# Optimization experiments

Measured on AMD Instinct MI355X. Metric: run time of the kernel, lower is better.

## Reference

```python
import jax, jax.numpy as jnp
import numpy as np

THETA = 10000.0


def apply_rope(t):
    """Partial rotary on first head_dim//2 dims, interleaved pairs (rotary_embedding_torch).
    t: (B, H, S, D) float32."""
    B, H, S, D = t.shape
    rot_dim = D // 2  # RotaryEmbedding(head_dim // 2)
    inv_freq = 1.0 / (THETA ** (jnp.arange(0, rot_dim, 2, dtype=jnp.float32) / rot_dim))  # (rot_dim//2,)
    pos = jnp.arange(S, dtype=jnp.float32)
    freqs = pos[:, None] * inv_freq[None, :]            # (S, rot_dim//2)
    freqs = jnp.repeat(freqs, 2, axis=-1)               # (S, rot_dim) interleaved
    cos, sin = jnp.cos(freqs), jnp.sin(freqs)           # (S, rot_dim)
    t_rot, t_pass = t[..., :rot_dim], t[..., rot_dim:]
    x1 = t_rot[..., 0::2]
    x2 = t_rot[..., 1::2]
    rot_half = jnp.stack((-x2, x1), axis=-1).reshape(t_rot.shape)
    t_rot = t_rot * cos + rot_half * sin
    return jnp.concatenate([t_rot, t_pass], axis=-1)


def setup_inputs() -> dict:
    key = jax.random.key(0)
    k1, k2, k3, k4, k5 = jax.random.split(key, 5)
    B, S, Dm = 2, 2048, 1024
    scale = 1.0 / np.sqrt(Dm)
    return {
        "x": jax.random.normal(k1, (B, S, Dm), dtype=jnp.float32),
        "Wqkv": jax.random.normal(k2, (3 * Dm, Dm), dtype=jnp.float32) * scale,
        "bqkv": jax.random.normal(k3, (3 * Dm,), dtype=jnp.float32) * 0.01,
        "Wout": jax.random.normal(k4, (Dm, Dm), dtype=jnp.float32) * scale,
        "bout": jax.random.normal(k5, (Dm,), dtype=jnp.float32) * 0.01,
    }


def reference(x, Wqkv, bqkv, Wout, bout):
    B, S, Dm = x.shape
    H = 16
    Dh = Dm // H
    qkv = x @ Wqkv.T + bqkv                              # (B, S, 3*Dm)
    qkv = qkv.reshape(B, S, 3, H, Dh).transpose(2, 0, 3, 1, 4)  # (3, B, H, S, Dh)
    q, k, v = qkv[0], qkv[1], qkv[2]
    q = apply_rope(q.astype(jnp.float32))
    k = apply_rope(k.astype(jnp.float32))
    scores = jnp.einsum("bhqd,bhkd->bhqk", q, k) / jnp.sqrt(jnp.float32(Dh))
    attn = jax.nn.softmax(scores, axis=-1)
    out = jnp.einsum("bhqk,bhkd->bhqd", attn, v)         # (B, H, S, Dh)
    out = out.transpose(0, 2, 1, 3).reshape(B, S, Dm)
    return out @ Wout.T + bout
```

## Files before the change

kernel.cpp:

```cpp
#include <hip/hip_runtime.h>

#define S_LEN 2048
#define DMODEL 1024
#define NHEAD 16
#define DHEAD 64
#define BATCH 2
#define BH_TOT (BATCH * NHEAD)
#define TOK (BATCH * S_LEN)
#define NQKV (3 * DMODEL)

#define QSCALE 0.18033688011112042f

typedef float  f32x4  __attribute__((ext_vector_type(4)));
typedef float  f32x16 __attribute__((ext_vector_type(16)));
typedef int    i32x4  __attribute__((ext_vector_type(4)));
typedef unsigned u32x2 __attribute__((ext_vector_type(2)));
typedef __bf16 bf16x8 __attribute__((ext_vector_type(8)));
typedef __bf16 bf16x4 __attribute__((ext_vector_type(4)));
typedef __bf16 bf16x2 __attribute__((ext_vector_type(2)));

typedef __attribute__((address_space(1))) void* as1_ptr;
typedef __attribute__((address_space(3))) void* as3_ptr;

__device__ __forceinline__ void gl2lds16(const void* g, void* l) {
  __builtin_amdgcn_global_load_lds((as1_ptr)(void*)g, (as3_ptr)l, 16, 0, 0);
}

__device__ __forceinline__ f32x4 mfma32(bf16x8 a, bf16x8 b, f32x4 c) {
  return __builtin_amdgcn_mfma_f32_16x16x32_bf16(a, b, c, 0, 0, 0);
}

__device__ __forceinline__ f32x16 mfma3216(bf16x8 a, bf16x8 b, f32x16 c) {
  return __builtin_amdgcn_mfma_f32_32x32x16_bf16(a, b, c, 0, 0, 0);
}

__device__ __forceinline__ unsigned pack2(float a, float b) {
  bf16x2 t;
  t[0] = (__bf16)a;
  t[1] = (__bf16)b;
  return __builtin_bit_cast(unsigned, t);
}

__device__ __forceinline__ bf16x8 pfragn(float a0, float a1, float a2, float a3,
                                         float a4, float a5, float a6, float a7) {
  const i32x4 w = {(int)pack2(a0, a1), (int)pack2(a2, a3),
                   (int)pack2(a4, a5), (int)pack2(a6, a7)};
  return __builtin_bit_cast(bf16x8, w);
}

__global__ __launch_bounds__(256) void cvt_kernel(const float* __restrict__ src,
                                                  __bf16* __restrict__ dst, int n) {
  const int i = (blockIdx.x * 256 + threadIdx.x) * 4;
  if (i >= n) return;
  const f32x4 v = *(const f32x4*)(src + i);
  bf16x4 o;
  o[0] = (__bf16)v[0]; o[1] = (__bf16)v[1]; o[2] = (__bf16)v[2]; o[3] = (__bf16)v[3];
  *(bf16x4*)(dst + i) = o;
}

__device__ __forceinline__ void gemm_tile_128(const __bf16* __restrict__ A,
                                              const __bf16* __restrict__ Bw,
                                              const int Kd, const int tileM, const int tileN,
                                              __bf16* As, __bf16* Bs, f32x4 acc[4][4]) {
  const int t    = threadIdx.x;
  const int lane = t & 63;
  const int wave = t >> 6;
  const int quad = lane >> 4;
  const int c    = lane & 15;
  const int wm   = (wave >> 1) << 6;
  const int wn   = (wave & 1) << 6;

  const int u0 = t, u1 = t + 256;
  const __bf16* gA0 = A  + (size_t)(tileM + (u0 >> 2)) * Kd + (u0 & 3) * 8;
  const __bf16* gA1 = A  + (size_t)(tileM + (u1 >> 2)) * Kd + (u1 & 3) * 8;
  const __bf16* gB0 = Bw + (size_t)(tileN + (u0 >> 2)) * Kd + (u0 & 3) * 8;
  const __bf16* gB1 = Bw + (size_t)(tileN + (u1 >> 2)) * Kd + (u1 & 3) * 8;
  __bf16* lA0 = As + u0 * 8; __bf16* lA1 = As + u1 * 8;
  __bf16* lB0 = Bs + u0 * 8; __bf16* lB1 = Bs + u1 * 8;

  for (int k0 = 0; k0 < Kd; k0 += 32) {
    gl2lds16(gA0 + k0, lA0);
    gl2lds16(gA1 + k0, lA1);
    gl2lds16(gB0 + k0, lB0);
    gl2lds16(gB1 + k0, lB1);
    __syncthreads();
    bf16x8 af[4], bfr[4];
#pragma unroll
    for (int mt = 0; mt < 4; ++mt)
      af[mt] = *(const bf16x8*)(As + (wm + mt * 16 + c) * 32 + quad * 8);
#pragma unroll
    for (int nt = 0; nt < 4; ++nt)
      bfr[nt] = *(const bf16x8*)(Bs + (wn + nt * 16 + c) * 32 + quad * 8);
#pragma unroll
    for (int mt = 0; mt < 4; ++mt)
#pragma unroll
      for (int nt = 0; nt < 4; ++nt)
        acc[mt][nt] = mfma32(af[mt], bfr[nt], acc[mt][nt]);
    __syncthreads();
  }
}

__global__ __launch_bounds__(256) void gemm_qkv_kernel(const __bf16* __restrict__ xb,
                                                       const __bf16* __restrict__ Wb,
                                                       const float* __restrict__ bias,
                                                       __bf16* __restrict__ Qb,
                                                       __bf16* __restrict__ Kb,
                                                       __bf16* __restrict__ Vtb) {
  __shared__ __align__(16) __bf16 As[128 * 32];
  __shared__ __align__(16) __bf16 Bs[128 * 32];
  f32x4 acc[4][4];
#pragma unroll
  for (int i = 0; i < 4; ++i)
#pragma unroll
    for (int j = 0; j < 4; ++j) acc[i][j] = (f32x4){0.f, 0.f, 0.f, 0.f};

  const int tileM = blockIdx.y * 128;
  const int tileN = blockIdx.x * 128;
  gemm_tile_128(xb, Wb, DMODEL, tileM, tileN, As, Bs, acc);

  const int t = threadIdx.x;
  const int lane = t & 63, wave = t >> 6;
  const int quad = lane >> 4, c = lane & 15;
  const int wm = (wave >> 1) << 6, wn = (wave & 1) << 6;

#pragma unroll
  for (int nt = 0; nt < 4; ++nt) {
    const int col = tileN + wn + nt * 16 + c;
    const float bv = bias[col];
    const int which = col >> 10;
    const int h  = (col >> 6) & 15;
    const int dh = col & 63;
    if (which == 2) {
#pragma unroll
      for (int mt = 0; mt < 4; ++mt) {
        const int row0 = tileM + wm + mt * 16 + quad * 4;
        const int bb = row0 >> 11;
        const int ss = row0 & (S_LEN - 1);
        bf16x4 o;
#pragma unroll
        for (int r = 0; r < 4; ++r) o[r] = (__bf16)(acc[mt][nt][r] + bv);
        *(bf16x4*)(Vtb + (((size_t)(bb * NHEAD + h)) * DHEAD + dh) * S_LEN + ss) = o;
      }
    } else {
      __bf16* dst = (which == 0) ? Qb : Kb;
      const float scl = (which == 0) ? QSCALE : 1.0f;
#pragma unroll
      for (int mt = 0; mt < 4; ++mt) {
#pragma unroll
        for (int r = 0; r < 4; ++r) {
          const int row = tileM + wm + mt * 16 + quad * 4 + r;
          const int bb = row >> 11;
          const int ss = row & (S_LEN - 1);
          dst[(((size_t)(bb * NHEAD + h)) * S_LEN + ss) * DHEAD + dh] =
              (__bf16)((acc[mt][nt][r] + bv) * scl);
        }
      }
    }
  }
}

__global__ __launch_bounds__(256) void gemm_out_kernel(const __bf16* __restrict__ AOb,
                                                       const __bf16* __restrict__ Wb,
                                                       const float* __restrict__ bout,
                                                       float* __restrict__ out) {
  __shared__ __align__(16) __bf16 As[128 * 32];
  __shared__ __align__(16) __bf16 Bs[128 * 32];
  f32x4 acc[4][4];
#pragma unroll
  for (int i = 0; i < 4; ++i)
#pragma unroll
    for (int j = 0; j < 4; ++j) acc[i][j] = (f32x4){0.f, 0.f, 0.f, 0.f};

  const int tileM = blockIdx.y * 128;
  const int tileN = blockIdx.x * 128;
  gemm_tile_128(AOb, Wb, DMODEL, tileM, tileN, As, Bs, acc);

  const int t = threadIdx.x;
  const int lane = t & 63, wave = t >> 6;
  const int quad = lane >> 4, c = lane & 15;
  const int wm = (wave >> 1) << 6, wn = (wave & 1) << 6;

#pragma unroll
  for (int nt = 0; nt < 4; ++nt) {
    const int col = tileN + wn + nt * 16 + c;
    const float bv = bout[col];
#pragma unroll
    for (int mt = 0; mt < 4; ++mt) {
#pragma unroll
      for (int r = 0; r < 4; ++r) {
        const int row = tileM + wm + mt * 16 + quad * 4 + r;
        out[(size_t)row * DMODEL + col] = acc[mt][nt][r] + bv;
      }
    }
  }
}

__global__ __launch_bounds__(256) void rope_kernel(__bf16* __restrict__ Qb, __bf16* __restrict__ Kb) {
  const int idx = blockIdx.x * 256 + threadIdx.x;
  const int j  = idx & 15;
  const int s  = (idx >> 4) & (S_LEN - 1);
  const int bh = (idx >> 15) & (BH_TOT - 1);
  __bf16* base = (idx >> 20) ? Kb : Qb;
  bf16x2* p = (bf16x2*)(base + ((size_t)bh * S_LEN + s) * DHEAD) + j;
  bf16x2 v = *p;
  const float x1 = (float)v[0];
  const float x2 = (float)v[1];
  const float LOG2_10000 = 13.287712379549449f;
  const float inv = exp2f(-(float)j * (LOG2_10000 / 16.0f));
  const float ang = (float)s * inv;
  float sn, cs;
  sincosf(ang, &sn, &cs);
  bf16x2 o;
  o[0] = (__bf16)(x1 * cs - x2 * sn);
  o[1] = (__bf16)(x2 * cs + x1 * sn);
  *p = o;
}

__global__ __launch_bounds__(128, 2) void attn_kernel(const __bf16* __restrict__ Qb,
                                                      const __bf16* __restrict__ Kb,
                                                      const __bf16* __restrict__ Vtb,
                                                      __bf16* __restrict__ AOb) {
  __shared__ __align__(16) __bf16 Ks[2][64 * 64];
  __shared__ __align__(16) __bf16 Vts[2][64 * 64];

  const int qt = blockIdx.x;
  const int bh = blockIdx.y;
  const int b = bh >> 4, h = bh & 15;
  const int t = threadIdx.x, wave = t >> 6, lane = t & 63;
  const int c31 = lane & 31, hi = lane >> 5;
  const int cx = c31 & 7;
  const size_t head = (size_t)bh * S_LEN * DHEAD;
  const int q0w = qt * 64 + wave * 32;

  bf16x8 qf[4];
#pragma unroll
  for (int s = 0; s < 4; ++s)
    qf[s] = *(const bf16x8*)(Qb + head + (size_t)(q0w + c31) * DHEAD + s * 16 + hi * 8);

  f32x16 zzero;
#pragma unroll
  for (int i = 0; i < 16; ++i) zzero[i] = 0.f;

  f32x16 ota[2], otb[2];
  ota[0] = zzero; ota[1] = zzero; otb[0] = zzero; otb[1] = zzero;
  float lp = 0.f;

  const __bf16* kg[4];
  const __bf16* vg[4];
  int loff[4];
#pragma unroll
  for (int i = 0; i < 4; ++i) {
    const int u = t + 128 * i;
    const int r = u >> 3, ch = (u & 7) ^ (r & 7);
    kg[i] = Kb + head + (size_t)r * DHEAD + ch * 8;
    vg[i] = Vtb + ((size_t)bh * DHEAD + r) * S_LEN + ch * 8;
    loff[i] = u * 8;
  }

#pragma unroll
  for (int i = 0; i < 4; ++i) {
    gl2lds16(kg[i], &Ks[0][loff[i]]);
    gl2lds16(vg[i], &Vts[0][loff[i]]);
  }

#define VREAD64(db, cb)                                                                   \
  __builtin_bit_cast(bf16x8, (i32x4){                                                     \
      (int)__builtin_bit_cast(u32x2, *(const bf16x4*)(&Vts[cur][((db)*32 + c31) * 64 +    \
                                  (((cb) ^ cx) * 8) + hi * 4]))[0],                       \
      (int)__builtin_bit_cast(u32x2, *(const bf16x4*)(&Vts[cur][((db)*32 + c31) * 64 +    \
                                  (((cb) ^ cx) * 8) + hi * 4]))[1],                       \
      (int)__builtin_bit_cast(u32x2, *(const bf16x4*)(&Vts[cur][((db)*32 + c31) * 64 +    \
                                  ((((cb) + 1) ^ cx) * 8) + hi * 4]))[0],                 \
      (int)__builtin_bit_cast(u32x2, *(const bf16x4*)(&Vts[cur][((db)*32 + c31) * 64 +    \
                                  ((((cb) + 1) ^ cx) * 8) + hi * 4]))[1]})

  for (int kb = 0; kb < S_LEN / 64; ++kb) {
    __syncthreads();
    const int cur = kb & 1;
    if (kb + 1 < S_LEN / 64) {
      const int nxt = cur ^ 1;
      const int k0n = (kb + 1) * 64;
#pragma unroll
      for (int i = 0; i < 4; ++i) {
        gl2lds16(kg[i] + (size_t)k0n * DHEAD, &Ks[nxt][loff[i]]);
        gl2lds16(vg[i] + k0n, &Vts[nxt][loff[i]]);
      }
    }

    bf16x8 kA0[4], kA1[4];
#pragma unroll
    for (int s = 0; s < 4; ++s) {
      kA0[s] = *(const bf16x8*)(&Ks[cur][c31 * 64 + (((s * 2 + hi) ^ cx) * 8)]);
      kA1[s] = *(const bf16x8*)(&Ks[cur][(32 + c31) * 64 + (((s * 2 + hi) ^ cx) * 8)]);
    }

    f32x16 z0 = zzero, z1 = zzero;
    __builtin_amdgcn_s_setprio(1);
#pragma unroll
    for (int s = 0; s < 4; ++s) {
      z0 = mfma3216(kA0[s], qf[s], z0);
      z1 = mfma3216(kA1[s], qf[s], z1);
    }
    __builtin_amdgcn_s_setprio(0);

    float p0[16], p1[16];
#pragma unroll
    for (int r = 0; r < 16; ++r) p0[r] = __builtin_amdgcn_exp2f(z0[r]);
#pragma unroll
    for (int r = 0; r < 16; ++r) p1[r] = __builtin_amdgcn_exp2f(z1[r]);

    lp += (((p0[0] + p0[1]) + (p0[2] + p0[3])) + ((p0[4] + p0[5]) + (p0[6] + p0[7])))
        + (((p0[8] + p0[9]) + (p0[10] + p0[11])) + ((p0[12] + p0[13]) + (p0[14] + p0[15])));
    lp += (((p1[0] + p1[1]) + (p1[2] + p1[3])) + ((p1[4] + p1[5]) + (p1[6] + p1[7])))
        + (((p1[8] + p1[9]) + (p1[10] + p1[11])) + ((p1[12] + p1[13]) + (p1[14] + p1[15])));

    __builtin_amdgcn_s_setprio(1);
    {
      const bf16x8 f0 = pfragn(p0[0], p0[1], p0[2], p0[3], p0[4], p0[5], p0[6], p0[7]);
      ota[0] = mfma3216(VREAD64(0, 0), f0, ota[0]);
      ota[1] = mfma3216(VREAD64(1, 0), f0, ota[1]);
      const bf16x8 f1 = pfragn(p0[8], p0[9], p0[10], p0[11], p0[12], p0[13], p0[14], p0[15]);
      otb[0] = mfma3216(VREAD64(0, 2), f1, otb[0]);
      otb[1] = mfma3216(VREAD64(1, 2), f1, otb[1]);
    }
    {
      const bf16x8 f0 = pfragn(p1[0], p1[1], p1[2], p1[3], p1[4], p1[5], p1[6], p1[7]);
      ota[0] = mfma3216(VREAD64(0, 4), f0, ota[0]);
      ota[1] = mfma3216(VREAD64(1, 4), f0, ota[1]);
      const bf16x8 f1 = pfragn(p1[8], p1[9], p1[10], p1[11], p1[12], p1[13], p1[14], p1[15]);
      otb[0] = mfma3216(VREAD64(0, 6), f1, otb[0]);
      otb[1] = mfma3216(VREAD64(1, 6), f1, otb[1]);
    }
    __builtin_amdgcn_s_setprio(0);
  }
#undef VREAD64

#pragma unroll
  for (int i = 0; i < 16; ++i) { ota[0][i] += otb[0][i]; ota[1][i] += otb[1][i]; }
  const float l = lp + __shfl_xor(lp, 32);
  const float inv = 1.0f / l;
  const int q = q0w + c31;
#pragma unroll
  for (int db = 0; db < 2; ++db) {
#pragma unroll
    for (int rg = 0; rg < 4; ++rg) {
      bf16x4 o;
#pragma unroll
      for (int i = 0; i < 4; ++i) o[i] = (__bf16)(ota[db][rg * 4 + i] * inv);
      const int d0 = db * 32 + rg * 8 + hi * 4;
      *(bf16x4*)(AOb + ((size_t)(b * S_LEN + q)) * DMODEL + h * DHEAD + d0) = o;
    }
  }
}

extern "C" void kernel_launch(void* const* d_in, const int* in_sizes, int n_in,
                              void* d_out, int out_size, void* d_ws, size_t ws_size,
                              hipStream_t stream) {
  const float* x    = (const float*)d_in[0];
  const float* Wqkv = (const float*)d_in[1];
  const float* bqkv = (const float*)d_in[2];
  const float* Wout = (const float*)d_in[3];
  const float* bout = (const float*)d_in[4];
  float* out = (float*)d_out;

  char* ws = (char*)d_ws;
  __bf16* xb    = (__bf16*)(ws + 0);
  __bf16* Wqkvb = (__bf16*)(ws + (size_t)8  * 1024 * 1024);
  __bf16* Woutb = (__bf16*)(ws + (size_t)14 * 1024 * 1024);
  __bf16* Qb    = (__bf16*)(ws + (size_t)16 * 1024 * 1024);
  __bf16* Kb    = (__bf16*)(ws + (size_t)24 * 1024 * 1024);
  __bf16* Vtb   = (__bf16*)(ws + (size_t)32 * 1024 * 1024);
  __bf16* AOb   = (__bf16*)(ws + (size_t)40 * 1024 * 1024);

  cvt_kernel<<<(TOK * DMODEL) / 1024, 256, 0, stream>>>(x, xb, TOK * DMODEL);
  cvt_kernel<<<(NQKV * DMODEL) / 1024, 256, 0, stream>>>(Wqkv, Wqkvb, NQKV * DMODEL);
  cvt_kernel<<<(DMODEL * DMODEL) / 1024, 256, 0, stream>>>(Wout, Woutb, DMODEL * DMODEL);

  gemm_qkv_kernel<<<dim3(NQKV / 128, TOK / 128), 256, 0, stream>>>(xb, Wqkvb, bqkv, Qb, Kb, Vtb);

  rope_kernel<<<(2 * BH_TOT * S_LEN * 16) / 256, 256, 0, stream>>>(Qb, Kb);

  attn_kernel<<<dim3(S_LEN / 64, BH_TOT), 128, 0, stream>>>(Qb, Kb, Vtb, AOb);

  gemm_out_kernel<<<dim3(DMODEL / 128, TOK / 128), 256, 0, stream>>>(AOb, Woutb, bout, out);
}
```

Measured before the change: 200.1 us.

## Restructure attention to single-wave blocks with 32-key tiles and no barriers

The attention kernel now runs one 64-thread wave per block over 32 queries, and processes keys in 32-row tiles instead of 64. Because each block is a single wave, __syncthreads is replaced by an explicit vmcnt wait, and the K and V fragments are read into registers before the next tile's async loads are issued into the other buffer. This removes cross-wave barrier stalls and doubles the number of blocks, which may improve latency hiding. The cost is half the K/V reuse per global load across queries, so L2 traffic doubles, along with more loop iterations and a new V swizzle pattern.

```diff
diff --git a/kernel.cpp b/kernel.cpp
--- a/kernel.cpp
+++ b/kernel.cpp
@@ -216,21 +216,22 @@
   *p = o;
 }
 
-__global__ __launch_bounds__(128, 2) void attn_kernel(const __bf16* __restrict__ Qb,
-                                                      const __bf16* __restrict__ Kb,
-                                                      const __bf16* __restrict__ Vtb,
-                                                      __bf16* __restrict__ AOb) {
-  __shared__ __align__(16) __bf16 Ks[2][64 * 64];
-  __shared__ __align__(16) __bf16 Vts[2][64 * 64];
+__global__ __launch_bounds__(64, 2) void attn_kernel(const __bf16* __restrict__ Qb,
+                                                     const __bf16* __restrict__ Kb,
+                                                     const __bf16* __restrict__ Vtb,
+                                                     __bf16* __restrict__ AOb) {
+  __shared__ __align__(16) __bf16 Ks[2][32 * 64];
+  __shared__ __align__(16) __bf16 Vts[2][64 * 32];
 
   const int qt = blockIdx.x;
   const int bh = blockIdx.y;
   const int b = bh >> 4, h = bh & 15;
-  const int t = threadIdx.x, wave = t >> 6, lane = t & 63;
+  const int lane = threadIdx.x & 63;
   const int c31 = lane & 31, hi = lane >> 5;
-  const int cx = c31 & 7;
+  const int cx7 = c31 & 7;
+  const int cxv = (c31 >> 1) & 3;
   const size_t head = (size_t)bh * S_LEN * DHEAD;
-  const int q0w = qt * 64 + wave * 32;
+  const int q0w = qt * 32;
 
   bf16x8 qf[4];
 #pragma unroll
@@ -247,93 +248,84 @@
 
   const __bf16* kg[4];
   const __bf16* vg[4];
-  int loff[4];
+  int lofK[4], lofV[4];
 #pragma unroll
   for (int i = 0; i < 4; ++i) {
-    const int u = t + 128 * i;
-    const int r = u >> 3, ch = (u & 7) ^ (r & 7);
-    kg[i] = Kb + head + (size_t)r * DHEAD + ch * 8;
-    vg[i] = Vtb + ((size_t)bh * DHEAD + r) * S_LEN + ch * 8;
-    loff[i] = u * 8;
+    const int u = lane + 64 * i;
+    const int rk = u >> 3, ck = (u & 7) ^ (rk & 7);
+    kg[i] = Kb + head + (size_t)rk * DHEAD + ck * 8;
+    lofK[i] = u * 8;
+    const int rv = u >> 2, cv = (u & 3) ^ ((rv >> 1) & 3);
+    vg[i] = Vtb + ((size_t)bh * DHEAD + rv) * S_LEN + cv * 8;
+    lofV[i] = u * 8;
   }
 
 #pragma unroll
   for (int i = 0; i < 4; ++i) {
-    gl2lds16(kg[i], &Ks[0][loff[i]]);
-    gl2lds16(vg[i], &Vts[0][loff[i]]);
-  }
-
-#define VREAD64(db, cb)                                                                   \
-  __builtin_bit_cast(bf16x8, (i32x4){                                                     \
-      (int)__builtin_bit_cast(u32x2, *(const bf16x4*)(&Vts[cur][((db)*32 + c31) * 64 +    \
-                                  (((cb) ^ cx) * 8) + hi * 4]))[0],                       \
-      (int)__builtin_bit_cast(u32x2, *(const bf16x4*)(&Vts[cur][((db)*32 + c31) * 64 +    \
-                                  (((cb) ^ cx) * 8) + hi * 4]))[1],                       \
-      (int)__builtin_bit_cast(u32x2, *(const bf16x4*)(&Vts[cur][((db)*32 + c31) * 64 +    \
-                                  ((((cb) + 1) ^ cx) * 8) + hi * 4]))[0],                 \
-      (int)__builtin_bit_cast(u32x2, *(const bf16x4*)(&Vts[cur][((db)*32 + c31) * 64 +    \
-                                  ((((cb) + 1) ^ cx) * 8) + hi * 4]))[1]})
-
-  for (int kb = 0; kb < S_LEN / 64; ++kb) {
-    __syncthreads();
-    const int cur = kb & 1;
-    if (kb + 1 < S_LEN / 64) {
-      const int nxt = cur ^ 1;
-      const int k0n = (kb + 1) * 64;
-#pragma unroll
-      for (int i = 0; i < 4; ++i) {
-        gl2lds16(kg[i] + (size_t)k0n * DHEAD, &Ks[nxt][loff[i]]);
-        gl2lds16(vg[i] + k0n, &Vts[nxt][loff[i]]);
-      }
-    }
-
-    bf16x8 kA0[4], kA1[4];
-#pragma unroll
-    for (int s = 0; s < 4; ++s) {
-      kA0[s] = *(const bf16x8*)(&Ks[cur][c31 * 64 + (((s * 2 + hi) ^ cx) * 8)]);
-      kA1[s] = *(const bf16x8*)(&Ks[cur][(32 + c31) * 64 + (((s * 2 + hi) ^ cx) * 8)]);
-    }
-
-    f32x16 z0 = zzero, z1 = zzero;
-    __builtin_amdgcn_s_setprio(1);
-#pragma unroll
-    for (int s = 0; s < 4; ++s) {
-      z0 = mfma3216(kA0[s], qf[s], z0);
-      z1 = mfma3216(kA1[s], qf[s], z1);
-    }
-    __builtin_amdgcn_s_setprio(0);
-
-    float p0[16], p1[16];
-#pragma unroll
-    for (int r = 0; r < 16; ++r) p0[r] = __builtin_amdgcn_exp2f(z0[r]);
-#pragma unroll
-    for (int r = 0; r < 16; ++r) p1[r] = __builtin_amdgcn_exp2f(z1[r]);
-
-    lp += (((p0[0] + p0[1]) + (p0[2] + p0[3])) + ((p0[4] + p0[5]) + (p0[6] + p0[7])))
-        + (((p0[8] + p0[9]) + (p0[10] + p0[11])) + ((p0[12] + p0[13]) + (p0[14] + p0[15])));
-    lp += (((p1[0] + p1[1]) + (p1[2] + p1[3])) + ((p1[4] + p1[5]) + (p1[6] + p1[7])))
-        + (((p1[8] + p1[9]) + (p1[10] + p1[11])) + ((p1[12] + p1[13]) + (p1[14] + p1[15])));
-
-    __builtin_amdgcn_s_setprio(1);
-    {
-      const bf16x8 f0 = pfragn(p0[0], p0[1], p0[2], p0[3], p0[4], p0[5], p0[6], p0[7]);
-      ota[0] = mfma3216(VREAD64(0, 0), f0, ota[0]);
-      ota[1] = mfma3216(VREAD64(1, 0), f0, ota[1]);
-      const bf16x8 f1 = pfragn(p0[8], p0[9], p0[10], p0[11], p0[12], p0[13], p0[14], p0[15]);
-      otb[0] = mfma3216(VREAD64(0, 2), f1, otb[0]);
-      otb[1] = mfma3216(VREAD64(1, 2), f1, otb[1]);
-    }
-    {
-      const bf16x8 f0 = pfragn(p1[0], p1[1], p1[2], p1[3], p1[4], p1[5], p1[6], p1[7]);
-      ota[0] = mfma3216(VREAD64(0, 4), f0, ota[0]);
-      ota[1] = mfma3216(VREAD64(1, 4), f0, ota[1]);
-      const bf16x8 f1 = pfragn(p1[8], p1[9], p1[10], p1[11], p1[12], p1[13], p1[14], p1[15]);
-      otb[0] = mfma3216(VREAD64(0, 6), f1, otb[0]);
-      otb[1] = mfma3216(VREAD64(1, 6), f1, otb[1]);
-    }
-    __builtin_amdgcn_s_setprio(0);
-  }
-#undef VREAD64
+    gl2lds16(kg[i], &Ks[0][lofK[i]]);
+    gl2lds16(vg[i], &Vts[0][lofV[i]]);
+  }
+
+#define VFRAG(CUR, db, kc)                                                                 \
+  __builtin_bit_cast(bf16x8, (i32x4){                                                      \
+      (int)__builtin_bit_cast(u32x2, *(const bf16x4*)(&Vts[CUR][((db) * 32 + c31) * 32 +   \
+                                     ((((kc) * 2) ^ cxv) * 8) + hi * 4]))[0],              \
+      (int)__builtin_bit_cast(u32x2, *(const bf16x4*)(&Vts[CUR][((db) * 32 + c31) * 32 +   \
+                                     ((((kc) * 2) ^ cxv) * 8) + hi * 4]))[1],              \
+      (int)__builtin_bit_cast(u32x2, *(const bf16x4*)(&Vts[CUR][((db) * 32 + c31) * 32 +   \
+                                     ((((kc) * 2 + 1) ^ cxv) * 8) + hi * 4]))[0],          \
+      (int)__builtin_bit_cast(u32x2, *(const bf16x4*)(&Vts[CUR][((db) * 32 + c31) * 32 +   \
+                                     ((((kc) * 2 + 1) ^ cxv) * 8) + hi * 4]))[1]})
+
+#define ATTN_TILE(KB, CUR)                                                                 \
+  {                                                                                        \
+    asm volatile("s_waitcnt vmcnt(0)" ::: "memory");                                       \
+    __builtin_amdgcn_sched_barrier(0);                                                     \
+    bf16x8 kA[4];                                                                          \
+    _Pragma("unroll")                                                                      \
+    for (int s = 0; s < 4; ++s)                                                            \
+      kA[s] = *(const bf16x8*)(&Ks[CUR][c31 * 64 + (((s * 2 + hi) ^ cx7) * 8)]);           \
+    const bf16x8 vA00 = VFRAG(CUR, 0, 0);                                                  \
+    const bf16x8 vA10 = VFRAG(CUR, 1, 0);                                                  \
+    const bf16x8 vA01 = VFRAG(CUR, 0, 1);                                                  \
+    const bf16x8 vA11 = VFRAG(CUR, 1, 1);                                                  \
+    __builtin_amdgcn_sched_barrier(0);                                                     \
+    if ((KB) + 1 < S_LEN / 32) {                                                           \
+      const int ka = ((KB) + 1) * (32 * DHEAD);                                            \
+      const int va = ((KB) + 1) * 32;                                                      \
+      _Pragma("unroll")                                                                    \
+      for (int i = 0; i < 4; ++i) {                                                        \
+        gl2lds16(kg[i] + ka, &Ks[(CUR) ^ 1][lofK[i]]);                                     \
+        gl2lds16(vg[i] + va, &Vts[(CUR) ^ 1][lofV[i]]);                                    \
+      }                                                                                    \
+    }                                                                                      \
+    __builtin_amdgcn_sched_barrier(0);                                                     \
+    f32x16 z = zzero;                                                                      \
+    __builtin_amdgcn_s_setprio(1);                                                         \
+    _Pragma("unroll")                                                                      \
+    for (int s = 0; s < 4; ++s) z = mfma3216(kA[s], qf[s], z);                             \
+    __builtin_amdgcn_s_setprio(0);                                                         \
+    float p[16];                                                                           \
+    _Pragma("unroll")                                                                      \
+    for (int r = 0; r < 16; ++r) p[r] = __builtin_amdgcn_exp2f(z[r]);                      \
+    lp += (((p[0] + p[1]) + (p[2] + p[3])) + ((p[4] + p[5]) + (p[6] + p[7])))              \
+        + (((p[8] + p[9]) + (p[10] + p[11])) + ((p[12] + p[13]) + (p[14] + p[15])));       \
+    const bf16x8 f0 = pfragn(p[0], p[1], p[2], p[3], p[4], p[5], p[6], p[7]);              \
+    const bf16x8 f1 = pfragn(p[8], p[9], p[10], p[11], p[12], p[13], p[14], p[15]);        \
+    __builtin_amdgcn_s_setprio(1);                                                         \
+    ota[0] = mfma3216(vA00, f0, ota[0]);                                                   \
+    ota[1] = mfma3216(vA10, f0, ota[1]);                                                   \
+    otb[0] = mfma3216(vA01, f1, otb[0]);                                                   \
+    otb[1] = mfma3216(vA11, f1, otb[1]);                                                   \
+    __builtin_amdgcn_s_setprio(0);                                                         \
+  }
+
+  for (int kbb = 0; kbb < S_LEN / 64; ++kbb) {
+    ATTN_TILE(2 * kbb, 0)
+    ATTN_TILE(2 * kbb + 1, 1)
+  }
+#undef ATTN_TILE
+#undef VFRAG
 
 #pragma unroll
   for (int i = 0; i < 16; ++i) { ota[0][i] += otb[0][i]; ota[1][i] += otb[1][i]; }
@@ -380,7 +372,7 @@
 
   rope_kernel<<<(2 * BH_TOT * S_LEN * 16) / 256, 256, 0, stream>>>(Qb, Kb);
 
-  attn_kernel<<<dim3(S_LEN / 64, BH_TOT), 128, 0, stream>>>(Qb, Kb, Vtb, AOb);
+  attn_kernel<<<dim3(S_LEN / 32, BH_TOT), 64, 0, stream>>>(Qb, Kb, Vtb, AOb);
 
   gemm_out_kernel<<<dim3(DMODEL / 128, TOK / 128), 256, 0, stream>>>(AOb, Woutb, bout, out);
 }
```

Result: slower. 212.0 us (+6.0%).

## Double-buffer GEMM LDS tiles and merge three conversion kernels into one

Applied to the files above, without the earlier changes.

The shared 128x128 GEMM tile loop now uses two LDS buffers. The next K-slice's global-to-LDS load is issued before computing on the current slice, and one barrier per step is removed, so load latency can overlap with MFMA work. The three fp32-to-bf16 conversion launches are merged into one kernel that picks its source by index range, cutting launch overhead. LDS use per block doubles, which may reduce occupancy, and the overlap depends on the async load ordering staying correct with a single barrier per stage.

```diff
diff --git a/kernel.cpp b/kernel.cpp
--- a/kernel.cpp
+++ b/kernel.cpp
@@ -48,20 +48,33 @@
   return __builtin_bit_cast(bf16x8, w);
 }
 
-__global__ __launch_bounds__(256) void cvt_kernel(const float* __restrict__ src,
-                                                  __bf16* __restrict__ dst, int n) {
+__global__ __launch_bounds__(256) void cvt3_kernel(const float* __restrict__ x,
+                                                   const float* __restrict__ w1,
+                                                   const float* __restrict__ w2,
+                                                   __bf16* __restrict__ xb,
+                                                   __bf16* __restrict__ w1b,
+                                                   __bf16* __restrict__ w2b) {
   const int i = (blockIdx.x * 256 + threadIdx.x) * 4;
-  if (i >= n) return;
-  const f32x4 v = *(const f32x4*)(src + i);
+  const int N0 = TOK * DMODEL;
+  const int N1 = NQKV * DMODEL;
+  const float* src;
+  __bf16* dst;
+  int off;
+  if (i < N0)            { src = x;  dst = xb;  off = i; }
+  else if (i < N0 + N1)  { src = w1; dst = w1b; off = i - N0; }
+  else                   { src = w2; dst = w2b; off = i - N0 - N1; }
+  const f32x4 v = *(const f32x4*)(src + off);
   bf16x4 o;
   o[0] = (__bf16)v[0]; o[1] = (__bf16)v[1]; o[2] = (__bf16)v[2]; o[3] = (__bf16)v[3];
-  *(bf16x4*)(dst + i) = o;
-}
-
+  *(bf16x4*)(dst + off) = o;
+}
+
+template <int KSTEPS>
 __device__ __forceinline__ void gemm_tile_128(const __bf16* __restrict__ A,
                                               const __bf16* __restrict__ Bw,
                                               const int Kd, const int tileM, const int tileN,
-                                              __bf16* As, __bf16* Bs, f32x4 acc[4][4]) {
+                                              __bf16* As0, __bf16* As1,
+                                              __bf16* Bs0, __bf16* Bs1, f32x4 acc[4][4]) {
   const int t    = threadIdx.x;
   const int lane = t & 63;
   const int wave = t >> 6;
@@ -75,29 +88,42 @@
   const __bf16* gA1 = A  + (size_t)(tileM + (u1 >> 2)) * Kd + (u1 & 3) * 8;
   const __bf16* gB0 = Bw + (size_t)(tileN + (u0 >> 2)) * Kd + (u0 & 3) * 8;
   const __bf16* gB1 = Bw + (size_t)(tileN + (u1 >> 2)) * Kd + (u1 & 3) * 8;
-  __bf16* lA0 = As + u0 * 8; __bf16* lA1 = As + u1 * 8;
-  __bf16* lB0 = Bs + u0 * 8; __bf16* lB1 = Bs + u1 * 8;
-
-  for (int k0 = 0; k0 < Kd; k0 += 32) {
-    gl2lds16(gA0 + k0, lA0);
-    gl2lds16(gA1 + k0, lA1);
-    gl2lds16(gB0 + k0, lB0);
-    gl2lds16(gB1 + k0, lB1);
+
+#define G_STAGE(K0, AS, BS)                  \
+  {                                          \
+    gl2lds16(gA0 + (K0), (AS) + u0 * 8);     \
+    gl2lds16(gA1 + (K0), (AS) + u1 * 8);     \
+    gl2lds16(gB0 + (K0), (BS) + u0 * 8);     \
+    gl2lds16(gB1 + (K0), (BS) + u1 * 8);     \
+  }
+
+#define G_COMPUTE(AS, BS)                                                      \
+  {                                                                            \
+    bf16x8 af[4], bfr[4];                                                      \
+    _Pragma("unroll")                                                          \
+    for (int mt = 0; mt < 4; ++mt)                                             \
+      af[mt] = *(const bf16x8*)((AS) + (wm + mt * 16 + c) * 32 + quad * 8);    \
+    _Pragma("unroll")                                                          \
+    for (int nt = 0; nt < 4; ++nt)                                             \
+      bfr[nt] = *(const bf16x8*)((BS) + (wn + nt * 16 + c) * 32 + quad * 8);   \
+    _Pragma("unroll")                                                          \
+    for (int mt = 0; mt < 4; ++mt)                                             \
+      _Pragma("unroll")                                                        \
+      for (int nt = 0; nt < 4; ++nt)                                           \
+        acc[mt][nt] = mfma32(af[mt], bfr[nt], acc[mt][nt]);                    \
+  }
+
+  G_STAGE(0, As0, Bs0);
+  for (int kk = 0; kk < KSTEPS; kk += 2) {
     __syncthreads();
-    bf16x8 af[4], bfr[4];
-#pragma unroll
-    for (int mt = 0; mt < 4; ++mt)
-      af[mt] = *(const bf16x8*)(As + (wm + mt * 16 + c) * 32 + quad * 8);
-#pragma unroll
-    for (int nt = 0; nt < 4; ++nt)
-      bfr[nt] = *(const bf16x8*)(Bs + (wn + nt * 16 + c) * 32 + quad * 8);
-#pragma unroll
-    for (int mt = 0; mt < 4; ++mt)
-#pragma unroll
-      for (int nt = 0; nt < 4; ++nt)
-        acc[mt][nt] = mfma32(af[mt], bfr[nt], acc[mt][nt]);
+    if (kk + 1 < KSTEPS) G_STAGE((kk + 1) * 32, As1, Bs1);
+    G_COMPUTE(As0, Bs0);
     __syncthreads();
-  }
+    if (kk + 2 < KSTEPS) G_STAGE((kk + 2) * 32, As0, Bs0);
+    G_COMPUTE(As1, Bs1);
+  }
+#undef G_STAGE
+#undef G_COMPUTE
 }
 
 __global__ __launch_bounds__(256) void gemm_qkv_kernel(const __bf16* __restrict__ xb,
@@ -106,8 +132,8 @@
                                                        __bf16* __restrict__ Qb,
                                                        __bf16* __restrict__ Kb,
                                                        __bf16* __restrict__ Vtb) {
-  __shared__ __align__(16) __bf16 As[128 * 32];
-  __shared__ __align__(16) __bf16 Bs[128 * 32];
+  __shared__ __align__(16) __bf16 As[2][128 * 32];
+  __shared__ __align__(16) __bf16 Bs[2][128 * 32];
   f32x4 acc[4][4];
 #pragma unroll
   for (int i = 0; i < 4; ++i)
@@ -116,7 +142,7 @@
 
   const int tileM = blockIdx.y * 128;
   const int tileN = blockIdx.x * 128;
-  gemm_tile_128(xb, Wb, DMODEL, tileM, tileN, As, Bs, acc);
+  gemm_tile_128<DMODEL / 32>(xb, Wb, DMODEL, tileM, tileN, As[0], As[1], Bs[0], Bs[1], acc);
 
   const int t = threadIdx.x;
   const int lane = t & 63, wave = t >> 6;
@@ -163,8 +189,8 @@
                                                        const __bf16* __restrict__ Wb,
                                                        const float* __restrict__ bout,
                                                        float* __restrict__ out) {
-  __shared__ __align__(16) __bf16 As[128 * 32];
-  __shared__ __align__(16) __bf16 Bs[128 * 32];
+  __shared__ __align__(16) __bf16 As[2][128 * 32];
+  __shared__ __align__(16) __bf16 Bs[2][128 * 32];
   f32x4 acc[4][4];
 #pragma unroll
   for (int i = 0; i < 4; ++i)
@@ -173,7 +199,7 @@
 
   const int tileM = blockIdx.y * 128;
   const int tileN = blockIdx.x * 128;
-  gemm_tile_128(AOb, Wb, DMODEL, tileM, tileN, As, Bs, acc);
+  gemm_tile_128<DMODEL / 32>(AOb, Wb, DMODEL, tileM, tileN, As[0], As[1], Bs[0], Bs[1], acc);
 
   const int t = threadIdx.x;
   const int lane = t & 63, wave = t >> 6;
@@ -372,9 +398,8 @@
   __bf16* Vtb   = (__bf16*)(ws + (size_t)32 * 1024 * 1024);
   __bf16* AOb   = (__bf16*)(ws + (size_t)40 * 1024 * 1024);
 
-  cvt_kernel<<<(TOK * DMODEL) / 1024, 256, 0, stream>>>(x, xb, TOK * DMODEL);
-  cvt_kernel<<<(NQKV * DMODEL) / 1024, 256, 0, stream>>>(Wqkv, Wqkvb, NQKV * DMODEL);
-  cvt_kernel<<<(DMODEL * DMODEL) / 1024, 256, 0, stream>>>(Wout, Woutb, DMODEL * DMODEL);
+  cvt3_kernel<<<(TOK * DMODEL + NQKV * DMODEL + DMODEL * DMODEL) / 1024, 256, 0, stream>>>(
+      x, Wqkv, Wout, xb, Wqkvb, Woutb);
 
   gemm_qkv_kernel<<<dim3(NQKV / 128, TOK / 128), 256, 0, stream>>>(xb, Wqkvb, bqkv, Qb, Kb, Vtb);
 
```

Measured after the change: 201.7 us. About the same (+0.8%).
